# Kernel tuning notes

Measured on AMD Instinct MI355X. Metric: run time of the kernel, lower is better.

Reference implementation:

```python
import jax, jax.numpy as jnp
import numpy as np
import math

B, QLEN, KLEN = 8, 128, 1024
KDIM = QDIM = ADIM = ODIM = 512
HM, HC = 4, 4            # monotonic / chunkwise heads
CHUNK = 4                # chunkwise attention window
EPS = 1e-6
SHARPENING = 1.0
NEG_INF = float(np.finfo(np.float32).min)


def moving_sum(x, back, forward):
    """Windowed sum over last axis: out[k] = sum_{j=k-back}^{k+forward} x[j].
    Equivalent to the conv1d-with-ones-filter moving_sum in the torch code."""
    K = x.shape[-1]
    xp = jnp.pad(x, [(0, 0)] * (x.ndim - 1) + [(back, forward)])
    cs = jnp.cumsum(xp, axis=-1)
    L = back + forward + 1
    upper = jax.lax.slice_in_dim(cs, L - 1, L - 1 + K, axis=-1)
    lower = jnp.concatenate([jnp.zeros_like(cs[..., :1]),
                             jax.lax.slice_in_dim(cs, 0, K - 1, axis=-1)], axis=-1)
    return upper - lower


def safe_cumprod(x, eps):
    """exp(exclusive_cumsum(log(clip(x, eps, 1)))) along last axis."""
    logx = jnp.log(jnp.clip(x, eps, 1.0))
    excl = jnp.concatenate([jnp.zeros_like(logx[..., :1]),
                            jnp.cumsum(logx, axis=-1)[..., :-1]], axis=-1)
    return jnp.exp(excl)


def _heads(x, w, b, h):
    y = x @ w + b                                   # [B, L, ADIM]
    bs, L, _ = y.shape
    return y.reshape(bs, L, h, -1).transpose(0, 2, 1, 3)  # [B, h, L, d_k]


def setup_inputs() -> dict:
    key = jax.random.key(0)
    ks = jax.random.split(key, 16)
    s = 0.02
    f32 = jnp.float32
    return {
        "key_x": jax.random.normal(ks[0], (B, KLEN, KDIM), f32),
        "query_x": jax.random.normal(ks[1], (B, QLEN, QDIM), f32),
        "mask": jnp.ones((B, QLEN, KLEN), jnp.int32),
        "wk_m": jax.random.normal(ks[2], (KDIM, ADIM), f32) * s,
        "bk_m": jnp.zeros((ADIM,), f32),
        "wq_m": jax.random.normal(ks[3], (QDIM, ADIM), f32) * s,
        "bq_m": jnp.zeros((ADIM,), f32),
        "r": jnp.asarray(-4.0, f32),
        "wk_c": jax.random.normal(ks[4], (KDIM, ADIM), f32) * s,
        "bk_c": jnp.zeros((ADIM,), f32),
        "wq_c": jax.random.normal(ks[5], (QDIM, ADIM), f32) * s,
        "bq_c": jnp.zeros((ADIM,), f32),
        "wv": jax.random.normal(ks[6], (KDIM, ADIM), f32) * s,
        "bv": jnp.zeros((ADIM,), f32),
        "wo": jax.random.normal(ks[7], (ADIM, ODIM), f32) * s,
        "bo": jnp.zeros((ODIM,), f32),
    }


def reference(key_x, query_x, mask, wk_m, bk_m, wq_m, bq_m, r,
              wk_c, bk_c, wq_c, bq_c, wv, bv, wo, bo):
    scale = math.sqrt(ADIM)
    m = (mask[:, None] > 0)                                    # [B,1,Q,K]

    # ---- monotonic energy (scaled_dot + offset r) ----
    km = _heads(key_x, wk_m, bk_m, HM)                         # [B,HM,K,dk]
    qm = _heads(query_x, wq_m, bq_m, HM)                       # [B,HM,Q,dk]
    e_mono = jnp.einsum('bhqd,bhkd->bhqk', qm, km) / scale + r
    e_mono = jnp.where(m, e_mono, NEG_INF)

    # ---- monotonic alpha via safe_cumprod + per-step cumsum recurrence ----
    p_choose = jax.nn.sigmoid(e_mono)                          # [B,HM,Q,K]
    cp = safe_cumprod(1.0 - p_choose, EPS)                     # [B,HM,Q,K]
    aw0 = jnp.zeros((B, HM, KLEN), e_mono.dtype).at[..., 0].set(1.0)

    def step(aw_prev, pc):
        p_i, cp_i = pc                                         # [B,HM,K]
        aw = p_i * cp_i * jnp.cumsum(aw_prev / jnp.maximum(cp_i, EPS), axis=-1)
        return aw, aw

    _, alpha = jax.lax.scan(step, aw0,
                            (p_choose.transpose(2, 0, 1, 3),
                             cp.transpose(2, 0, 1, 3)))
    alpha = alpha.transpose(1, 2, 0, 3)                        # [B,HM,Q,K]

    # ---- chunkwise energy ----
    kc = _heads(key_x, wk_c, bk_c, HC)
    qc = _heads(query_x, wq_c, bq_c, HC)
    e_chunk = jnp.einsum('bhqd,bhkd->bhqk', qc, kc) / scale
    e_chunk = jnp.where(m, e_chunk, NEG_INF)

    # ---- efficient chunkwise attention (clipped-logit trick) ----
    e = e_chunk - jnp.max(e_chunk, axis=-1, keepdims=True)
    sexp = jnp.maximum(jnp.exp(e), 1e-5)[:, None]              # [B,1,HC,Q,K]
    denom = moving_sum(sexp, CHUNK - 1, 0)                     # [B,1,HC,Q,K]
    beta = sexp * moving_sum(alpha[:, :, None] * SHARPENING / denom,
                             0, CHUNK - 1)                     # [B,HM,HC,Q,K]
    beta = beta.reshape(B, HM * HC, QLEN, KLEN)

    # ---- context + output projection ----
    v = (key_x @ wv + bv).reshape(B, KLEN, HM * HC, ADIM // (HM * HC))
    cv = jnp.einsum('bhqk,bkhd->bqhd', beta, v).reshape(B, QLEN, ADIM)
    return cv @ wo + bo
```

## Files before the change

kernel.cpp:

```cpp
#include <hip/hip_runtime.h>
#include <hip/hip_bf16.h>


#define NEG_INF (-3.402823466e38f)
#define EPS_MOCHA 1e-6f
#define INV_SCALE 0.04419417382415922f

typedef _Float16 half8 __attribute__((ext_vector_type(8)));
typedef _Float16 half4v __attribute__((ext_vector_type(4)));
typedef float f32x4 __attribute__((ext_vector_type(4)));

#define WAITBAR(N) asm volatile("s_waitcnt vmcnt(" #N ") lgkmcnt(0)\n\ts_barrier" ::: "memory")
#define BARLG() asm volatile("s_waitcnt lgkmcnt(0)\n\ts_barrier" ::: "memory")

__device__ __forceinline__ float frcp(float x) { return __builtin_amdgcn_rcpf(x); }

__device__ __forceinline__ float wave_incl_scan(float x)
{
    int v;
    v = __builtin_amdgcn_update_dpp(0, __builtin_bit_cast(int, x), 0x111, 0xF, 0xF, false);
    x += __builtin_bit_cast(float, v);
    v = __builtin_amdgcn_update_dpp(0, __builtin_bit_cast(int, x), 0x112, 0xF, 0xF, false);
    x += __builtin_bit_cast(float, v);
    v = __builtin_amdgcn_update_dpp(0, __builtin_bit_cast(int, x), 0x114, 0xF, 0xF, false);
    x += __builtin_bit_cast(float, v);
    v = __builtin_amdgcn_update_dpp(0, __builtin_bit_cast(int, x), 0x118, 0xF, 0xF, false);
    x += __builtin_bit_cast(float, v);
    v = __builtin_amdgcn_update_dpp(0, __builtin_bit_cast(int, x), 0x142, 0xA, 0xF, false);
    x += __builtin_bit_cast(float, v);
    v = __builtin_amdgcn_update_dpp(0, __builtin_bit_cast(int, x), 0x143, 0xC, 0xF, false);
    x += __builtin_bit_cast(float, v);
    return x;
}

__device__ __forceinline__ half8 cvt8(float4 a, float4 b)
{
    half8 h = {(_Float16)a.x, (_Float16)a.y, (_Float16)a.z, (_Float16)a.w,
               (_Float16)b.x, (_Float16)b.y, (_Float16)b.z, (_Float16)b.w};
    return h;
}

__global__ __launch_bounds__(256) void prep_all(
    const float* __restrict__ wk_m, const float* __restrict__ wk_c,
    const float* __restrict__ wv, const float* __restrict__ wq_m,
    const float* __restrict__ wq_c, const float* __restrict__ wo,
    const float* __restrict__ key_x, const float* __restrict__ query_x,
    const int* __restrict__ mask,
    _Float16* __restrict__ Wt5, _Float16* __restrict__ Wt_wo,
    _Float16* __restrict__ X16, signed char* __restrict__ mask8)
{
    __shared__ float T[64][65];
    const int bid = blockIdx.x;
    const int t = threadIdx.x;
    if (bid < 384) {
        const int z = bid >> 6, w = bid & 63;
        const float* W = (z == 0) ? wk_m : (z == 1) ? wk_c : (z == 2) ? wv
                       : (z == 3) ? wq_m : (z == 4) ? wq_c : wo;
        _Float16* O = (z < 5) ? (Wt5 + (size_t)z * 262144) : Wt_wo;
        const int n0 = (w & 7) * 64, k0 = (w >> 3) * 64;
        const int rr = t >> 4, cc = (t & 15) * 4;
#pragma unroll
        for (int r = 0; r < 4; ++r) {
            int k = r * 16 + rr;
            float4 v = *(const float4*)(W + (size_t)(k0 + k) * 512 + n0 + cc);
            T[k][cc + 0] = v.x; T[k][cc + 1] = v.y;
            T[k][cc + 2] = v.z; T[k][cc + 3] = v.w;
        }
        __syncthreads();
        const int nn = t >> 2, kc = (t & 3) * 16;
        _Float16 tmp[16];
#pragma unroll
        for (int i = 0; i < 16; ++i) tmp[i] = (_Float16)T[kc + i][nn];
        _Float16* Op = O + (size_t)(n0 + nn) * 512 + k0 + kc;
        *(half8*)(Op)     = *(half8*)&tmp[0];
        *(half8*)(Op + 8) = *(half8*)&tmp[8];
    } else if (bid < 2688) {
        const size_t KELEMS = (size_t)8192 * 512;
        size_t o = ((size_t)(bid - 384) * 256 + t) * 8;
        const float* s = (o < KELEMS) ? (key_x + o) : (query_x + (o - KELEMS));
        float4 a = *(const float4*)s;
        float4 b = *(const float4*)(s + 4);
        *(half8*)(X16 + o) = cvt8(a, b);
    } else {
        size_t o = ((size_t)(bid - 2688) * 256 + t) * 8;
        const int* mp = mask + o;
        int4 a = *(const int4*)mp;
        int4 b = *(const int4*)(mp + 4);
        unsigned long long pk = 0;
        pk |= (unsigned long long)(a.x != 0) << 0;
        pk |= (unsigned long long)(a.y != 0) << 8;
        pk |= (unsigned long long)(a.z != 0) << 16;
        pk |= (unsigned long long)(a.w != 0) << 24;
        pk |= (unsigned long long)(b.x != 0) << 32;
        pk |= (unsigned long long)(b.y != 0) << 40;
        pk |= (unsigned long long)(b.z != 0) << 48;
        pk |= (unsigned long long)(b.w != 0) << 56;
        *(unsigned long long*)(mask8 + o) = pk;
    }
}

__device__ __forceinline__ void stage16(const _Float16* src, _Float16* dst)
{
    __builtin_amdgcn_global_load_lds(
        (const __attribute__((address_space(1))) void*)src,
        (__attribute__((address_space(3))) void*)dst, 16, 0, 0);
}

template <int NSTEPS>
__device__ __forceinline__ void gemm8_f16(
    const _Float16* __restrict__ Abase, const _Float16* __restrict__ Bbase,
    _Float16* As, _Float16* Bs, f32x4 acc[4][2])
{
    const int tid = threadIdx.x;
    const int lane = tid & 63, wave = tid >> 6;
    const int wm = wave >> 2, wn = wave & 3;
    const int col = lane & 15, quad = lane >> 4;
    const int r0 = tid >> 2, seg = tid & 3;

    const _Float16* Ag = Abase + (size_t)r0 * 512 + seg * 8;
    const _Float16* Bg = Bbase + (size_t)r0 * 512 + seg * 8;

    stage16(Ag, As + tid * 8);
    stage16(Bg, Bs + tid * 8);
    if (NSTEPS > 1) {
        stage16(Ag + 32, As + 4096 + tid * 8);
        stage16(Bg + 32, Bs + 4096 + tid * 8);
        WAITBAR(2);
    } else {
        WAITBAR(0);
    }

#pragma unroll
    for (int ks = 0; ks < NSTEPS; ++ks) {
        const int cur = ks % 3;
        if (ks + 2 < NSTEPS) {
            const int s2 = (ks + 2) % 3;
            stage16(Ag + (ks + 2) * 32, As + s2 * 4096 + tid * 8);
            stage16(Bg + (ks + 2) * 32, Bs + s2 * 4096 + tid * 8);
        }
        const _Float16* Afr = As + cur * 4096 + (size_t)(wm * 64 + col) * 32 + quad * 8;
        const _Float16* Bfr = Bs + cur * 4096 + (size_t)(wn * 32 + col) * 32 + quad * 8;
        half8 a[4], b[2];
#pragma unroll
        for (int t = 0; t < 4; ++t) a[t] = *(const half8*)(Afr + (size_t)t * 16 * 32);
#pragma unroll
        for (int t = 0; t < 2; ++t) b[t] = *(const half8*)(Bfr + (size_t)t * 16 * 32);
#pragma unroll
        for (int mt = 0; mt < 4; ++mt)
#pragma unroll
            for (int nt = 0; nt < 2; ++nt)
                acc[mt][nt] = __builtin_amdgcn_mfma_f32_16x16x32_f16(
                    a[mt], b[nt], acc[mt][nt], 0, 0, 0);
        if (ks + 2 < NSTEPS)      WAITBAR(2);
        else if (ks + 1 < NSTEPS) WAITBAR(0);
    }
}

__device__ __forceinline__ void proj_epilogue8(
    f32x4 acc[4][2], const float* __restrict__ bias, void* __restrict__ Cv,
    int m0, int n0, int f16o)
{
    const int tid = threadIdx.x;
    const int lane = tid & 63, wave = tid >> 6;
    const int wm = wave >> 2, wn = wave & 3;
    const int col = lane & 15, quad = lane >> 4;
    float bnt[2];
#pragma unroll
    for (int nt = 0; nt < 2; ++nt)
        bnt[nt] = bias[n0 + wn * 32 + nt * 16 + col];
#pragma unroll
    for (int mt = 0; mt < 4; ++mt) {
        const int rowb = m0 + wm * 64 + mt * 16 + quad * 4;
#pragma unroll
        for (int nt = 0; nt < 2; ++nt) {
            const int cc = n0 + wn * 32 + nt * 16 + col;
#pragma unroll
            for (int r = 0; r < 4; ++r) {
                float v = acc[mt][nt][r] + bnt[nt];
                if (f16o)
                    ((_Float16*)Cv)[(size_t)(rowb + r) * 512 + cc] = (_Float16)v;
                else
                    ((float*)Cv)[(size_t)(rowb + r) * 512 + cc] = v;
            }
        }
    }
}

__global__ __launch_bounds__(512, 8) void mfma_proj5(
    const _Float16* __restrict__ X16, const _Float16* __restrict__ Wt5,
    const float* __restrict__ b0, void* __restrict__ C0,
    const float* __restrict__ b1, void* __restrict__ C1,
    const float* __restrict__ b2, void* __restrict__ C2,
    const float* __restrict__ b3, void* __restrict__ C3,
    const float* __restrict__ b4, void* __restrict__ C4)
{
    __shared__ _Float16 As[12288];
    __shared__ _Float16 Bs[12288];
    const int bid = (blockIdx.x & 7) * 104 + (blockIdx.x >> 3);
    int g, mblk, nblk;
    if (bid < 768) {
        g = bid >> 8; mblk = (bid & 255) >> 2; nblk = bid & 3;
    } else {
        const int t = bid - 768;
        g = 3 + (t >> 5); mblk = (t & 31) >> 2; nblk = t & 3;
    }
    const bool qry = g >= 3;
    const _Float16* A = X16 + (qry ? (size_t)8192 * 512 : 0);
    const _Float16* Wt = Wt5 + (size_t)g * 262144;
    const float* bias = (g == 0) ? b0 : (g == 1) ? b1 : (g == 2) ? b2
                      : (g == 3) ? b3 : b4;
    void* Cv = (g == 0) ? C0 : (g == 1) ? C1 : (g == 2) ? C2
             : (g == 3) ? C3 : C4;
    const int m0 = mblk * 128, n0 = nblk * 128;

    f32x4 acc[4][2];
#pragma unroll
    for (int mt = 0; mt < 4; ++mt)
#pragma unroll
        for (int nt = 0; nt < 2; ++nt) acc[mt][nt] = (f32x4)0.f;
    gemm8_f16<16>(A + (size_t)m0 * 512, Wt + (size_t)n0 * 512, As, Bs, acc);
    proj_epilogue8(acc, bias, Cv, m0, n0, 1);
}

__global__ __launch_bounds__(512, 4) void mfma_proj_out(
    const _Float16* __restrict__ A16, const _Float16* __restrict__ Wt,
    const float* __restrict__ bias, float* __restrict__ C)
{
    __shared__ _Float16 As[12288];
    __shared__ _Float16 Bs[12288];
    const int m0 = blockIdx.x * 128, n0 = blockIdx.y * 128;
    f32x4 acc[4][2];
#pragma unroll
    for (int mt = 0; mt < 4; ++mt)
#pragma unroll
        for (int nt = 0; nt < 2; ++nt) acc[mt][nt] = (f32x4)0.f;
    gemm8_f16<16>(A16 + (size_t)m0 * 512, Wt + (size_t)n0 * 512, As, Bs, acc);
    proj_epilogue8(acc, bias, C, m0, n0, 0);
}

__global__ __launch_bounds__(512, 4) void energy_mfma(
    const _Float16* __restrict__ Qm, const _Float16* __restrict__ Km,
    const _Float16* __restrict__ Qc, const _Float16* __restrict__ Kc,
    const signed char* __restrict__ mask8, float* __restrict__ e_mono,
    _Float16* __restrict__ e_chunk16, const float* __restrict__ r_ptr)
{
    __shared__ _Float16 As[12288];
    __shared__ _Float16 Bs[12288];
    const int tid = threadIdx.x;
    const int lane = tid & 63, wave = tid >> 6;
    const int wm = wave >> 2, wn = wave & 3;
    const int col = lane & 15, quad = lane >> 4;
    const int kt0 = blockIdx.x * 128;
    const int h = blockIdx.y;
    const int z = blockIdx.z;
    const int b = z & 7;
    const bool mono = z < 8;
    const _Float16* Qp = mono ? Qm : Qc;
    const _Float16* Kp = mono ? Km : Kc;
    const float rv = mono ? r_ptr[0] : 0.f;

    f32x4 acc[4][2];
#pragma unroll
    for (int mt = 0; mt < 4; ++mt)
#pragma unroll
        for (int nt = 0; nt < 2; ++nt) acc[mt][nt] = (f32x4)0.f;
    gemm8_f16<4>(Qp + (size_t)(b * 128) * 512 + h * 128,
                 Kp + (size_t)(b * 1024 + kt0) * 512 + h * 128, As, Bs, acc);

#pragma unroll
    for (int mt = 0; mt < 4; ++mt) {
        const int qb = wm * 64 + mt * 16 + quad * 4;
#pragma unroll
        for (int nt = 0; nt < 2; ++nt) {
            const int kc = kt0 + wn * 32 + nt * 16 + col;
#pragma unroll
            for (int r = 0; r < 4; ++r) {
                const int q = qb + r;
                const int mv = mask8[((size_t)b * 128 + q) * 1024 + kc];
                const size_t oi = (((size_t)b * 4 + h) * 128 + q) * 1024 + kc;
                float v = acc[mt][nt][r] * INV_SCALE + rv;
                if (mono) e_mono[oi] = mv ? v : NEG_INF;
                else      e_chunk16[oi] = (_Float16)(mv ? v : NEG_INF);
            }
        }
    }
}

__device__ __forceinline__ void transcend_row(
    const float* __restrict__ Erow, int lane, float o_pcp[16], float o_inv[16])
{
    const float* E = Erow + lane * 16;
    float e[16];
    *(float4*)&e[0]  = *(const float4*)(E);
    *(float4*)&e[4]  = *(const float4*)(E + 4);
    *(float4*)&e[8]  = *(const float4*)(E + 8);
    *(float4*)&e[12] = *(const float4*)(E + 12);

    float p[16], l[16];
#pragma unroll
    for (int i = 0; i < 16; ++i) {
        p[i] = frcp(1.f + __expf(-e[i]));
        l[i] = __logf(fmaxf(1.f - p[i], EPS_MOCHA));
    }
    float incl[16];
    incl[0] = l[0];
#pragma unroll
    for (int i = 1; i < 16; ++i) incl[i] = incl[i - 1] + l[i];
    float total = incl[15];
    float x = wave_incl_scan(total);
    float base = x - total;
#pragma unroll
    for (int i = 0; i < 16; ++i) {
        float cl = base + (i ? incl[i - 1] : 0.f);
        float cp = __expf(cl);
        o_pcp[i] = p[i] * cp;
        o_inv[i] = frcp(fmaxf(cp, EPS_MOCHA));
    }
}

#define SW2(k) ((k) + ((k) >> 4))

__global__ __launch_bounds__(512) void alpha_pre(
    const float* __restrict__ e_mono, float* __restrict__ G,
    float* __restrict__ pcp)
{
    __shared__ float pshare[8][1088];
    const int tid = threadIdx.x;
    const int lane = tid & 63;
    const int wid = tid >> 6;
    const int row = blockIdx.x * 8 + wid;
    const int q = row & 127;

    float pq[16], iq[16];
    transcend_row(e_mono + (size_t)row * 1024, lane, pq, iq);

    float* P = pcp + (size_t)row * 1024 + lane * 16;
    *(float4*)(P)      = *(float4*)&pq[0];
    *(float4*)(P + 4)  = *(float4*)&pq[4];
    *(float4*)(P + 8)  = *(float4*)&pq[8];
    *(float4*)(P + 12) = *(float4*)&pq[12];

#pragma unroll
    for (int i = 0; i < 16; ++i)
        pshare[wid][SW2(lane * 16 + i)] = pq[i];
    __syncthreads();

    float g[16];
    if (q == 0) {
#pragma unroll
        for (int i = 0; i < 16; ++i) g[i] = 0.f;
        if (lane == 0) g[0] = iq[0];
    } else if (wid > 0) {
#pragma unroll
        for (int i = 0; i < 16; ++i)
            g[i] = pshare[wid - 1][SW2(lane * 16 + i)] * iq[i];
    } else {
        float pm[16], im[16];
        transcend_row(e_mono + (size_t)(row - 1) * 1024, lane, pm, im);
#pragma unroll
        for (int i = 0; i < 16; ++i) g[i] = pm[i] * iq[i];
    }
    float* Gp = G + (size_t)row * 1024 + lane * 16;
    *(float4*)(Gp)      = *(float4*)&g[0];
    *(float4*)(Gp + 4)  = *(float4*)&g[4];
    *(float4*)(Gp + 8)  = *(float4*)&g[8];
    *(float4*)(Gp + 12) = *(float4*)&g[12];
}

__global__ __launch_bounds__(256) void alpha_scan(
    const float* __restrict__ G, float* __restrict__ S)
{
    __shared__ float carry[2][4];
    const int tid = threadIdx.x;
    const int lane = tid & 63, wid = tid >> 6;
    const int bh = blockIdx.x;
    const float* Gp = G + (size_t)bh * 131072 + tid * 4;
    float* Sp = S + (size_t)bh * 131072 + tid * 4;

    float4 g0 = *(const float4*)(Gp);
    float4 g1 = *(const float4*)(Gp + 1024);
    float4 g2 = *(const float4*)(Gp + 2048);
    float4 g3 = *(const float4*)(Gp + 3072);

    float Sv0 = 1.f, Sv1 = 1.f, Sv2 = 1.f, Sv3 = 1.f;

#define SCAN_STEP(GV, QQ)                                                    \
    {                                                                        \
        float i0 = GV.x * Sv0;                                               \
        float i1 = fmaf(GV.y, Sv1, i0);                                      \
        float i2 = fmaf(GV.z, Sv2, i1);                                      \
        float i3 = fmaf(GV.w, Sv3, i2);                                      \
        float x = wave_incl_scan(i3);                                        \
        float base = x - i3;                                                 \
        if (lane == 63) carry[(QQ) & 1][wid] = x;                            \
        BARLG();                                                             \
        float pre = 0.f;                                                     \
        if (wid > 0) pre += carry[(QQ) & 1][0];                              \
        if (wid > 1) pre += carry[(QQ) & 1][1];                              \
        if (wid > 2) pre += carry[(QQ) & 1][2];                              \
        float ba = pre + base;                                               \
        Sv0 = ba + i0; Sv1 = ba + i1; Sv2 = ba + i2; Sv3 = ba + i3;          \
        float4 sv = {Sv0, Sv1, Sv2, Sv3};                                    \
        *(float4*)(Sp + (size_t)(QQ) * 1024) = sv;                           \
    }

    for (int q = 0; q < 128; q += 4) {
        SCAN_STEP(g0, q);
        if (q + 4 < 128) g0 = *(const float4*)(Gp + (size_t)(q + 4) * 1024);
        SCAN_STEP(g1, q + 1);
        if (q + 5 < 128) g1 = *(const float4*)(Gp + (size_t)(q + 5) * 1024);
        SCAN_STEP(g2, q + 2);
        if (q + 6 < 128) g2 = *(const float4*)(Gp + (size_t)(q + 6) * 1024);
        SCAN_STEP(g3, q + 3);
        if (q + 7 < 128) g3 = *(const float4*)(Gp + (size_t)(q + 7) * 1024);
    }
#undef SCAN_STEP
}

__global__ __launch_bounds__(256) void beta_kernel(
    const _Float16* __restrict__ e_chunk16, const float* __restrict__ pcp,
    const float* __restrict__ S, _Float16* __restrict__ beta)
{
    __shared__ float red[4];
    __shared__ float edge_sx[4][4];
    __shared__ float edge_t[4][4][4];
    const int q = blockIdx.x, b = blockIdx.y;
    const int tid = threadIdx.x;
    const int lane = tid & 63, wid = tid >> 6;
    const int k4 = tid * 4;

    float av[4][4];
#pragma unroll
    for (int hm = 0; hm < 4; ++hm) {
        const size_t off = (((size_t)b * 4 + hm) * 128 + q) * 1024 + k4;
        float4 pv = *(const float4*)(pcp + off);
        float4 sv = *(const float4*)(S + off);
        av[hm][0] = pv.x * sv.x;
        av[hm][1] = pv.y * sv.y;
        av[hm][2] = pv.z * sv.z;
        av[hm][3] = pv.w * sv.w;
    }

    for (int hc = 0; hc < 4; ++hc) {
        half4v ev = *(const half4v*)(e_chunk16 + (((size_t)b * 4 + hc) * 128 + q) * 1024 + k4);
        float e[4] = {(float)ev[0], (float)ev[1], (float)ev[2], (float)ev[3]};

        float mx = fmaxf(fmaxf(e[0], e[1]), fmaxf(e[2], e[3]));
#pragma unroll
        for (int off = 32; off >= 1; off >>= 1)
            mx = fmaxf(mx, __shfl_xor(mx, off, 64));
        if (lane == 0) red[wid] = mx;
        __syncthreads();
        mx = fmaxf(fmaxf(red[0], red[1]), fmaxf(red[2], red[3]));

        float sx[4];
#pragma unroll
        for (int i = 0; i < 4; ++i)
            sx[i] = fmaxf(__expf(e[i] - mx), 1e-5f);
        if (lane == 63) {
            edge_sx[wid][0] = sx[0]; edge_sx[wid][1] = sx[1];
            edge_sx[wid][2] = sx[2]; edge_sx[wid][3] = sx[3];
        }
        __syncthreads();

        float p1 = __shfl_up(sx[3], 1, 64);
        float p2 = __shfl_up(sx[2], 1, 64);
        float p3 = __shfl_up(sx[1], 1, 64);
        if (lane == 0) {
            if (wid > 0) {
                p1 = edge_sx[wid - 1][3];
                p2 = edge_sx[wid - 1][2];
                p3 = edge_sx[wid - 1][1];
            } else {
                p1 = 0.f; p2 = 0.f; p3 = 0.f;
            }
        }
        float den[4];
        den[0] = sx[0] + p1 + p2 + p3;
        den[1] = sx[1] + sx[0] + p1 + p2;
        den[2] = sx[2] + sx[1] + sx[0] + p1;
        den[3] = sx[3] + sx[2] + sx[1] + sx[0];
        float rd[4];
#pragma unroll
        for (int i = 0; i < 4; ++i) rd[i] = frcp(den[i]);

        float t[4][4];
#pragma unroll
        for (int hm = 0; hm < 4; ++hm)
#pragma unroll
            for (int i = 0; i < 4; ++i)
                t[hm][i] = av[hm][i] * rd[i];
        if (lane == 0) {
#pragma unroll
            for (int hm = 0; hm < 4; ++hm) {
                edge_t[wid][hm][0] = t[hm][0]; edge_t[wid][hm][1] = t[hm][1];
                edge_t[wid][hm][2] = t[hm][2]; edge_t[wid][hm][3] = t[hm][3];
            }
        }
        __syncthreads();

#pragma unroll
        for (int hm = 0; hm < 4; ++hm) {
            float n1 = __shfl_down(t[hm][0], 1, 64);
            float n2 = __shfl_down(t[hm][1], 1, 64);
            float n3 = __shfl_down(t[hm][2], 1, 64);
            if (lane == 63) {
                if (wid < 3) {
                    n1 = edge_t[wid + 1][hm][0];
                    n2 = edge_t[wid + 1][hm][1];
                    n3 = edge_t[wid + 1][hm][2];
                } else {
                    n1 = 0.f; n2 = 0.f; n3 = 0.f;
                }
            }
            float o0 = sx[0] * (t[hm][0] + t[hm][1] + t[hm][2] + t[hm][3]);
            float o1 = sx[1] * (t[hm][1] + t[hm][2] + t[hm][3] + n1);
            float o2 = sx[2] * (t[hm][2] + t[hm][3] + n1 + n2);
            float o3 = sx[3] * (t[hm][3] + n1 + n2 + n3);
            _Float16* Brow = beta + (((size_t)b * 16 + hm * 4 + hc) * 128 + q) * 1024;
            half4v hv = {(_Float16)o0, (_Float16)o1, (_Float16)o2, (_Float16)o3};
            *(half4v*)(Brow + k4) = hv;
        }
    }
}

__global__ __launch_bounds__(512) void context_kernel(
    const _Float16* __restrict__ beta, const _Float16* __restrict__ V16,
    _Float16* __restrict__ cv16)
{
    __shared__ float bS[128][65];
    __shared__ float vS[128][36];
    const int qh = blockIdx.x, h = blockIdx.y, b = blockIdx.z;
    const int tid = threadIdx.x;
    const int ty = tid >> 3;
    const int tx = tid & 7;
    const int q0 = qh * 64;

    const _Float16* Bbase = beta + (((size_t)b * 16 + h) * 128 + q0) * 1024;
    const _Float16* Vbase = V16 + (size_t)b * 1024 * 512 + h * 32;

    float acc[4] = {0.f, 0.f, 0.f, 0.f};

    for (int k0 = 0; k0 < 1024; k0 += 128) {
        {
            const int r = tid >> 3, c = tid & 7;
            half8 v0 = *(const half8*)(Bbase + (size_t)r * 1024 + k0 + c * 16);
            half8 v1 = *(const half8*)(Bbase + (size_t)r * 1024 + k0 + c * 16 + 8);
#pragma unroll
            for (int j = 0; j < 8; ++j) {
                bS[c * 16 + j][r]     = (float)v0[j];
                bS[c * 16 + 8 + j][r] = (float)v1[j];
            }
        }
        {
            const int kk = tid >> 2, cc = tid & 3;
            half4v w0 = *(const half4v*)(Vbase + (size_t)(k0 + kk) * 512 + cc * 8);
            half4v w1 = *(const half4v*)(Vbase + (size_t)(k0 + kk) * 512 + cc * 8 + 4);
#pragma unroll
            for (int j = 0; j < 4; ++j) {
                vS[kk][cc * 8 + j]     = (float)w0[j];
                vS[kk][cc * 8 + 4 + j] = (float)w1[j];
            }
        }
        __syncthreads();
#pragma unroll 8
        for (int kk = 0; kk < 128; ++kk) {
            float a = bS[kk][ty];
            float bb[4];
            *(float4*)bb = *(const float4*)&vS[kk][tx * 4];
#pragma unroll
            for (int j = 0; j < 4; ++j) acc[j] = fmaf(a, bb[j], acc[j]);
        }
        __syncthreads();
    }
    _Float16* Cp = cv16 + ((size_t)b * 128 + q0 + ty) * 512 + h * 32 + tx * 4;
    half4v hv = {(_Float16)acc[0], (_Float16)acc[1],
                 (_Float16)acc[2], (_Float16)acc[3]};
    *(half4v*)Cp = hv;
}

extern "C" void kernel_launch(void* const* d_in, const int* in_sizes, int n_in,
                              void* d_out, int out_size, void* d_ws, size_t ws_size,
                              hipStream_t stream)
{
    const float* key_x   = (const float*)d_in[0];
    const float* query_x = (const float*)d_in[1];
    const int*   mask    = (const int*)d_in[2];
    const float* wk_m = (const float*)d_in[3];
    const float* bk_m = (const float*)d_in[4];
    const float* wq_m = (const float*)d_in[5];
    const float* bq_m = (const float*)d_in[6];
    const float* r    = (const float*)d_in[7];
    const float* wk_c = (const float*)d_in[8];
    const float* bk_c = (const float*)d_in[9];
    const float* wq_c = (const float*)d_in[10];
    const float* bq_c = (const float*)d_in[11];
    const float* wv   = (const float*)d_in[12];
    const float* bv   = (const float*)d_in[13];
    const float* wo   = (const float*)d_in[14];
    const float* bo   = (const float*)d_in[15];
    float* out = (float*)d_out;

    float* ws = (float*)d_ws;
    _Float16* hws = (_Float16*)d_ws;
    const size_t MEGF = 1024 * 1024;
    _Float16* Km16  = hws;
    _Float16* Kc16  = hws + 4 * MEGF;
    _Float16* Qm16  = hws + 8 * MEGF;
    _Float16* Qc16  = hws + 8 * MEGF + 524288;
    _Float16* X16   = hws + 16 * MEGF;
    signed char* mask8 = (signed char*)(hws + 20 * MEGF + MEGF / 2);
    float* e_mono  = ws + 11 * MEGF;
    _Float16* e_chunk16 = hws + 34 * MEGF;
    _Float16* V16  = hws + 38 * MEGF;
    float* G       = ws;
    float* pcp     = ws + 4 * MEGF;
    float* S       = ws + 23 * MEGF;
    _Float16* beta16 = hws + 16 * MEGF;
    _Float16* Wt5   = hws + 54 * MEGF;
    _Float16* Wt_wo = hws + 54 * MEGF + 5 * 262144;
    _Float16* cv16  = hws + 55 * MEGF + MEGF / 2;

    prep_all<<<dim3(3200), 256, 0, stream>>>(
        wk_m, wk_c, wv, wq_m, wq_c, wo, key_x, query_x, mask,
        Wt5, Wt_wo, X16, mask8);
    mfma_proj5<<<dim3(832), 512, 0, stream>>>(
        X16, Wt5, bk_m, Km16, bk_c, Kc16, bv, V16, bq_m, Qm16, bq_c, Qc16);
    energy_mfma<<<dim3(8, 4, 16), 512, 0, stream>>>(
        Qm16, Km16, Qc16, Kc16, mask8, e_mono, e_chunk16, r);
    alpha_pre<<<dim3(512), 512, 0, stream>>>(e_mono, G, pcp);
    alpha_scan<<<dim3(32), 256, 0, stream>>>(G, S);
    beta_kernel<<<dim3(128, 8), 256, 0, stream>>>(e_chunk16, pcp, S, beta16);
    context_kernel<<<dim3(2, 16, 8), 512, 0, stream>>>(beta16, V16, cv16);
    mfma_proj_out<<<dim3(8, 4), 512, 0, stream>>>(cv16, Wt_wo, bo, out);
}
```

Measured before the change: 243.8 us.

## Use MFMA for context GEMM and fold alpha product into scan

```diff
diff --git a/kernel.cpp b/kernel.cpp
--- a/kernel.cpp
+++ b/kernel.cpp
@@ -368,23 +368,29 @@
 }
 
 __global__ __launch_bounds__(256) void alpha_scan(
-    const float* __restrict__ G, float* __restrict__ S)
+    const float* __restrict__ G, const float* __restrict__ pcp,
+    float* __restrict__ alpha)
 {
     __shared__ float carry[2][4];
     const int tid = threadIdx.x;
     const int lane = tid & 63, wid = tid >> 6;
     const int bh = blockIdx.x;
     const float* Gp = G + (size_t)bh * 131072 + tid * 4;
-    float* Sp = S + (size_t)bh * 131072 + tid * 4;
+    const float* Pp = pcp + (size_t)bh * 131072 + tid * 4;
+    float* Ap = alpha + (size_t)bh * 131072 + tid * 4;
 
     float4 g0 = *(const float4*)(Gp);
     float4 g1 = *(const float4*)(Gp + 1024);
     float4 g2 = *(const float4*)(Gp + 2048);
     float4 g3 = *(const float4*)(Gp + 3072);
+    float4 p0 = *(const float4*)(Pp);
+    float4 p1 = *(const float4*)(Pp + 1024);
+    float4 p2 = *(const float4*)(Pp + 2048);
+    float4 p3 = *(const float4*)(Pp + 3072);
 
     float Sv0 = 1.f, Sv1 = 1.f, Sv2 = 1.f, Sv3 = 1.f;
 
-#define SCAN_STEP(GV, QQ)                                                    \
+#define SCAN_STEP(GV, PV, QQ)                                                \
     {                                                                        \
         float i0 = GV.x * Sv0;                                               \
         float i1 = fmaf(GV.y, Sv1, i0);                                      \
@@ -400,26 +406,38 @@
         if (wid > 2) pre += carry[(QQ) & 1][2];                              \
         float ba = pre + base;                                               \
         Sv0 = ba + i0; Sv1 = ba + i1; Sv2 = ba + i2; Sv3 = ba + i3;          \
-        float4 sv = {Sv0, Sv1, Sv2, Sv3};                                    \
-        *(float4*)(Sp + (size_t)(QQ) * 1024) = sv;                           \
+        float4 av = {PV.x * Sv0, PV.y * Sv1, PV.z * Sv2, PV.w * Sv3};        \
+        *(float4*)(Ap + (size_t)(QQ) * 1024) = av;                           \
     }
 
     for (int q = 0; q < 128; q += 4) {
-        SCAN_STEP(g0, q);
-        if (q + 4 < 128) g0 = *(const float4*)(Gp + (size_t)(q + 4) * 1024);
-        SCAN_STEP(g1, q + 1);
-        if (q + 5 < 128) g1 = *(const float4*)(Gp + (size_t)(q + 5) * 1024);
-        SCAN_STEP(g2, q + 2);
-        if (q + 6 < 128) g2 = *(const float4*)(Gp + (size_t)(q + 6) * 1024);
-        SCAN_STEP(g3, q + 3);
-        if (q + 7 < 128) g3 = *(const float4*)(Gp + (size_t)(q + 7) * 1024);
+        SCAN_STEP(g0, p0, q);
+        if (q + 4 < 128) {
+            g0 = *(const float4*)(Gp + (size_t)(q + 4) * 1024);
+            p0 = *(const float4*)(Pp + (size_t)(q + 4) * 1024);
+        }
+        SCAN_STEP(g1, p1, q + 1);
+        if (q + 5 < 128) {
+            g1 = *(const float4*)(Gp + (size_t)(q + 5) * 1024);
+            p1 = *(const float4*)(Pp + (size_t)(q + 5) * 1024);
+        }
+        SCAN_STEP(g2, p2, q + 2);
+        if (q + 6 < 128) {
+            g2 = *(const float4*)(Gp + (size_t)(q + 6) * 1024);
+            p2 = *(const float4*)(Pp + (size_t)(q + 6) * 1024);
+        }
+        SCAN_STEP(g3, p3, q + 3);
+        if (q + 7 < 128) {
+            g3 = *(const float4*)(Gp + (size_t)(q + 7) * 1024);
+            p3 = *(const float4*)(Pp + (size_t)(q + 7) * 1024);
+        }
     }
 #undef SCAN_STEP
 }
 
 __global__ __launch_bounds__(256) void beta_kernel(
-    const _Float16* __restrict__ e_chunk16, const float* __restrict__ pcp,
-    const float* __restrict__ S, _Float16* __restrict__ beta)
+    const _Float16* __restrict__ e_chunk16, const float* __restrict__ alpha,
+    _Float16* __restrict__ beta)
 {
     __shared__ float red[4];
     __shared__ float edge_sx[4][4];
@@ -433,12 +451,8 @@
 #pragma unroll
     for (int hm = 0; hm < 4; ++hm) {
         const size_t off = (((size_t)b * 4 + hm) * 128 + q) * 1024 + k4;
-        float4 pv = *(const float4*)(pcp + off);
-        float4 sv = *(const float4*)(S + off);
-        av[hm][0] = pv.x * sv.x;
-        av[hm][1] = pv.y * sv.y;
-        av[hm][2] = pv.z * sv.z;
-        av[hm][3] = pv.w * sv.w;
+        float4 a = *(const float4*)(alpha + off);
+        av[hm][0] = a.x; av[hm][1] = a.y; av[hm][2] = a.z; av[hm][3] = a.w;
     }
 
     for (int hc = 0; hc < 4; ++hc) {
@@ -524,59 +538,71 @@
     }
 }
 
-__global__ __launch_bounds__(512) void context_kernel(
+__global__ __launch_bounds__(256) void context_mfma(
     const _Float16* __restrict__ beta, const _Float16* __restrict__ V16,
     _Float16* __restrict__ cv16)
 {
-    __shared__ float bS[128][65];
-    __shared__ float vS[128][36];
+    __shared__ _Float16 As[2][64][72];
+    __shared__ _Float16 Bs[2][32][72];
     const int qh = blockIdx.x, h = blockIdx.y, b = blockIdx.z;
     const int tid = threadIdx.x;
-    const int ty = tid >> 3;
-    const int tx = tid & 7;
+    const int lane = tid & 63, wave = tid >> 6;
+    const int wm = wave >> 1, wn = wave & 1;
+    const int col = lane & 15, quad = lane >> 4;
     const int q0 = qh * 64;
 
-    const _Float16* Bbase = beta + (((size_t)b * 16 + h) * 128 + q0) * 1024;
-    const _Float16* Vbase = V16 + (size_t)b * 1024 * 512 + h * 32;
-
-    float acc[4] = {0.f, 0.f, 0.f, 0.f};
-
-    for (int k0 = 0; k0 < 1024; k0 += 128) {
-        {
-            const int r = tid >> 3, c = tid & 7;
-            half8 v0 = *(const half8*)(Bbase + (size_t)r * 1024 + k0 + c * 16);
-            half8 v1 = *(const half8*)(Bbase + (size_t)r * 1024 + k0 + c * 16 + 8);
-#pragma unroll
-            for (int j = 0; j < 8; ++j) {
-                bS[c * 16 + j][r]     = (float)v0[j];
-                bS[c * 16 + 8 + j][r] = (float)v1[j];
+    const int ar = tid >> 2, acs = tid & 3;
+    const _Float16* Ag = beta + (((size_t)b * 16 + h) * 128 + q0 + ar) * 1024 + acs * 16;
+    const int bk = tid >> 2, bds = tid & 3;
+    const _Float16* Vg = V16 + ((size_t)b * 1024 + bk) * 512 + h * 32 + bds * 8;
+
+    f32x4 acc[2];
+    acc[0] = (f32x4)0.f; acc[1] = (f32x4)0.f;
+
+    half8 ra0 = *(const half8*)(Ag);
+    half8 ra1 = *(const half8*)(Ag + 8);
+    half8 rv  = *(const half8*)(Vg);
+    *(half8*)&As[0][ar][acs * 16]     = ra0;
+    *(half8*)&As[0][ar][acs * 16 + 8] = ra1;
+#pragma unroll
+    for (int j = 0; j < 8; ++j) Bs[0][bds * 8 + j][bk] = rv[j];
+    BARLG();
+
+    for (int ks = 0; ks < 16; ++ks) {
+        const int cur = ks & 1, nxt = cur ^ 1;
+        if (ks + 1 < 16) {
+            const int k0 = (ks + 1) * 64;
+            ra0 = *(const half8*)(Ag + k0);
+            ra1 = *(const half8*)(Ag + k0 + 8);
+            rv  = *(const half8*)(Vg + (size_t)k0 * 512);
+        }
+#pragma unroll
+        for (int sub = 0; sub < 2; ++sub) {
+            half8 bf = *(const half8*)&Bs[cur][wn * 16 + col][sub * 32 + quad * 8];
+#pragma unroll
+            for (int mt = 0; mt < 2; ++mt) {
+                half8 af = *(const half8*)&As[cur][wm * 32 + mt * 16 + col][sub * 32 + quad * 8];
+                acc[mt] = __builtin_amdgcn_mfma_f32_16x16x32_f16(af, bf, acc[mt], 0, 0, 0);
             }
         }
-        {
-            const int kk = tid >> 2, cc = tid & 3;
-            half4v w0 = *(const half4v*)(Vbase + (size_t)(k0 + kk) * 512 + cc * 8);
-            half4v w1 = *(const half4v*)(Vbase + (size_t)(k0 + kk) * 512 + cc * 8 + 4);
-#pragma unroll
-            for (int j = 0; j < 4; ++j) {
-                vS[kk][cc * 8 + j]     = (float)w0[j];
-                vS[kk][cc * 8 + 4 + j] = (float)w1[j];
-            }
-        }
-        __syncthreads();
-#pragma unroll 8
-        for (int kk = 0; kk < 128; ++kk) {
-            float a = bS[kk][ty];
-            float bb[4];
-            *(float4*)bb = *(const float4*)&vS[kk][tx * 4];
-#pragma unroll
-            for (int j = 0; j < 4; ++j) acc[j] = fmaf(a, bb[j], acc[j]);
-        }
-        __syncthreads();
-    }
-    _Float16* Cp = cv16 + ((size_t)b * 128 + q0 + ty) * 512 + h * 32 + tx * 4;
-    half4v hv = {(_Float16)acc[0], (_Float16)acc[1],
-                 (_Float16)acc[2], (_Float16)acc[3]};
-    *(half4v*)Cp = hv;
+        if (ks + 1 < 16) {
+            *(half8*)&As[nxt][ar][acs * 16]     = ra0;
+            *(half8*)&As[nxt][ar][acs * 16 + 8] = ra1;
+#pragma unroll
+            for (int j = 0; j < 8; ++j) Bs[nxt][bds * 8 + j][bk] = rv[j];
+        }
+        BARLG();
+    }
+
+#pragma unroll
+    for (int mt = 0; mt < 2; ++mt) {
+        const int qb = q0 + wm * 32 + mt * 16 + quad * 4;
+#pragma unroll
+        for (int r = 0; r < 4; ++r) {
+            _Float16* Cp = cv16 + ((size_t)b * 128 + qb + r) * 512 + h * 32 + wn * 16 + col;
+            *Cp = (_Float16)acc[mt][r];
+        }
+    }
 }
 
 extern "C" void kernel_launch(void* const* d_in, const int* in_sizes, int n_in,
@@ -615,7 +641,7 @@
     _Float16* V16  = hws + 38 * MEGF;
     float* G       = ws;
     float* pcp     = ws + 4 * MEGF;
-    float* S       = ws + 23 * MEGF;
+    float* alpha   = ws + 23 * MEGF;
     _Float16* beta16 = hws + 16 * MEGF;
     _Float16* Wt5   = hws + 54 * MEGF;
     _Float16* Wt_wo = hws + 54 * MEGF + 5 * 262144;
@@ -629,8 +655,8 @@
     energy_mfma<<<dim3(8, 4, 16), 512, 0, stream>>>(
         Qm16, Km16, Qc16, Kc16, mask8, e_mono, e_chunk16, r);
     alpha_pre<<<dim3(512), 512, 0, stream>>>(e_mono, G, pcp);
-    alpha_scan<<<dim3(32), 256, 0, stream>>>(G, S);
-    beta_kernel<<<dim3(128, 8), 256, 0, stream>>>(e_chunk16, pcp, S, beta16);
-    context_kernel<<<dim3(2, 16, 8), 512, 0, stream>>>(beta16, V16, cv16);
+    alpha_scan<<<dim3(32), 256, 0, stream>>>(G, pcp, alpha);
+    beta_kernel<<<dim3(128, 8), 256, 0, stream>>>(e_chunk16, alpha, beta16);
+    context_mfma<<<dim3(2, 16, 8), 256, 0, stream>>>(beta16, V16, cv16);
     mfma_proj_out<<<dim3(8, 4), 512, 0, stream>>>(cv16, Wt_wo, bo, out);
 }
```

Result: faster. 218.6 us (median of 2 runs) (-10.3%).
